# Kernel tuning notes

Measured on AMD Instinct MI355X. Metric: run time of the kernel, lower is better.

Reference implementation:

```python
import jax, jax.numpy as jnp
import numpy as np

N_FEATURES = 1024
N_HEADS = 16
D_ATTN = 64


def setup_inputs() -> dict:
    key = jax.random.key(0)
    k_x, k_qkv, k_pw, k_pb = jax.random.split(key, 4)
    B, S = 2, 2048
    x = jax.random.normal(k_x, (B, S, N_FEATURES), dtype=jnp.float32)
    # torch nn.Linear weights are [out, in]; init scale ~ 1/sqrt(in)
    w_qkv = jax.random.normal(k_qkv, (3 * N_HEADS * D_ATTN, N_FEATURES), dtype=jnp.float32) / np.sqrt(N_FEATURES)
    w_proj = jax.random.normal(k_pw, (N_FEATURES, N_HEADS * D_ATTN), dtype=jnp.float32) / np.sqrt(N_HEADS * D_ATTN)
    b_proj = jax.random.normal(k_pb, (N_FEATURES,), dtype=jnp.float32) / np.sqrt(N_HEADS * D_ATTN)
    return {"x": x, "w_qkv": w_qkv, "w_proj": w_proj, "b_proj": b_proj}


def reference(x, w_qkv, w_proj, b_proj):
    B, S, F = x.shape
    H, D = N_HEADS, D_ATTN
    # fused QKV projection (bias=False): [B,S,3*H*D]
    qkv = jnp.einsum('bsf,of->bso', x, w_qkv)
    qkv = qkv.reshape(B, S, 3, H, D)
    q = jnp.transpose(qkv[:, :, 0], (0, 2, 1, 3))  # [B,H,S,D]
    k = jnp.transpose(qkv[:, :, 1], (0, 2, 1, 3))
    v = jnp.transpose(qkv[:, :, 2], (0, 2, 1, 3))
    scale = 1.0 / jnp.sqrt(jnp.asarray(D, dtype=x.dtype))
    scores = jnp.einsum('bhqd,bhkd->bhqk', q, k) * scale  # [B,H,S,S]
    attn = jax.nn.softmax(scores, axis=-1)
    out = jnp.einsum('bhqk,bhkd->bhqd', attn, v)  # [B,H,S,D]
    out = jnp.transpose(out, (0, 2, 1, 3)).reshape(B, S, H * D)
    # output projection (dropout is identity in eval mode)
    return jnp.einsum('bsm,fm->bsf', out, w_proj) + b_proj
```

## Files before the change

kernel.cpp:

```cpp
#include <hip/hip_runtime.h>
#include <hip/hip_bf16.h>
#include <math.h>

#define BATCH 2
#define SEQ 2048
#define NFEAT 1024
#define NHEAD 16
#define DHEAD 64
#define MROWS (BATCH * SEQ)
#define NQKV (3 * NHEAD * DHEAD)

typedef __attribute__((ext_vector_type(8))) short short8;
typedef __attribute__((ext_vector_type(4))) float floatx4;
typedef __attribute__((ext_vector_type(16))) float floatx16;
typedef __attribute__((ext_vector_type(4))) unsigned int uintx4;

#define CEXP 0.18033688f

__device__ __forceinline__ unsigned short f2bf(float f) {
    unsigned int u = __float_as_uint(f);
    u += 0x7fff + ((u >> 16) & 1);
    return (unsigned short)(u >> 16);
}

__device__ __forceinline__ float fast_exp2(float x) {
    return __builtin_amdgcn_exp2f(x);
}

__device__ __forceinline__ uint pack_bf16x2(float lo, float hi) {
    float2 t; t.x = lo; t.y = hi;
    __hip_bfloat162 h = __float22bfloat162_rn(t);
    union { __hip_bfloat162 h; uint u; } c; c.h = h;
    return c.u;
}

__device__ __forceinline__ void async16(const void* g, void* l) {
    __builtin_amdgcn_global_load_lds(
        (const __attribute__((address_space(1))) void*)g,
        (__attribute__((address_space(3))) void*)l, 16, 0, 0);
}

#define BAR_RAW() asm volatile("s_barrier" ::: "memory")
#define WAITV4()  { asm volatile("s_waitcnt vmcnt(4)" ::: "memory"); __builtin_amdgcn_sched_barrier(0); }
#define WAITV0()  { asm volatile("s_waitcnt vmcnt(0)" ::: "memory"); __builtin_amdgcn_sched_barrier(0); }

__global__ void cvt_swz(const float* __restrict__ x, const float* __restrict__ wq,
                        const float* __restrict__ wp,
                        ushort* __restrict__ xb, ushort* __restrict__ wqb,
                        ushort* __restrict__ wpb) {
    const int NX = MROWS * NFEAT / 4, NWQ = NQKV * NFEAT / 4, NWP = NFEAT * NFEAT / 4;
    int i = blockIdx.x * blockDim.x + threadIdx.x;
    if (i >= NX + NWQ + NWP) return;
    const float* src; ushort* dst; int idx4;
    if (i < NX)            { src = x;  dst = xb;  idx4 = i; }
    else if (i < NX + NWQ) { src = wq; dst = wqb; idx4 = i - NX; }
    else                   { src = wp; dst = wpb; idx4 = i - NX - NWQ; }
    float4 v = ((const float4*)src)[idx4];
    ushort4 o;
    o.x = f2bf(v.x); o.y = f2bf(v.y); o.z = f2bf(v.z); o.w = f2bf(v.w);
    const int e = idx4 * 4;
    const int k = e & (NFEAT - 1);
    const int row = e >> 10;
    const int kp = (k & ~31) | (((((k >> 3) & 3) ^ ((row >> 1) & 3))) << 3) | (k & 7);
    *(ushort4*)(dst + (size_t)row * NFEAT + kp) = o;
}

__global__ __launch_bounds__(256, 3)
void gemm_qkv(const ushort* __restrict__ A, const ushort* __restrict__ W,
              ushort* __restrict__ qb, ushort* __restrict__ kb, ushort* __restrict__ vtb) {
    __shared__ ushort smem[16384];
    ushort* As = smem;
    ushort* Bs = smem + 8192;
    const int tid = threadIdx.x;
    const int wave = tid >> 6, lane = tid & 63;
    const int id = blockIdx.x;
    const int xcd = id & 7, slot = id >> 3;
    const int by = (xcd >> 1) * 8 + slot / 12;
    const int bx = (xcd & 1) * 12 + slot % 12;
    const int m0 = by * 128, n0 = bx * 128;
    const int wm = (wave >> 1) * 64, wn = (wave & 1) * 64;
    const int lr = lane & 15, lg = lane >> 4;
    const int kswz = (lg ^ ((lr >> 1) & 3)) * 8;

    floatx4 acc[4][4] = {};

    for (int k0 = 0; k0 < NFEAT; k0 += 64) {
#pragma unroll
        for (int q = 0; q < 4; ++q) {
            const int s = q * 256 + tid;
            const int row = s >> 3, kc = (s & 7) * 8;
            async16(A + (size_t)(m0 + row) * NFEAT + k0 + kc, (void*)(As + s * 8));
            async16(W + (size_t)(n0 + row) * NFEAT + k0 + kc, (void*)(Bs + s * 8));
        }
        __syncthreads();
#pragma unroll
        for (int kk = 0; kk < 2; ++kk) {
            short8 a[4], b[4];
#pragma unroll
            for (int i = 0; i < 4; ++i)
                a[i] = *(const short8*)(As + (wm + i * 16 + lr) * 64 + kk * 32 + kswz);
#pragma unroll
            for (int j = 0; j < 4; ++j)
                b[j] = *(const short8*)(Bs + (wn + j * 16 + lr) * 64 + kk * 32 + kswz);
#pragma unroll
            for (int i = 0; i < 4; ++i)
#pragma unroll
                for (int j = 0; j < 4; ++j)
                    acc[i][j] = __builtin_amdgcn_mfma_f32_16x16x32_bf16(a[i], b[j], acc[i][j], 0, 0, 0);
        }
        __syncthreads();
    }

    const int t = n0 >> 10;
    const int bidx = m0 >> 11;
    if (t < 2) {
#pragma unroll
        for (int i = 0; i < 4; ++i)
#pragma unroll
            for (int j = 0; j < 4; ++j)
#pragma unroll
                for (int r = 0; r < 4; ++r) {
                    const int m = m0 + wm + i * 16 + lg * 4 + r;
                    const int n = n0 + wn + j * 16 + lr;
                    const int s = m & (SEQ - 1);
                    const int rem = n & 1023, h = rem >> 6, d = rem & 63;
                    if (t == 0) {
                        qb[((size_t)(bidx * NHEAD + h) * SEQ + s) * DHEAD + d] =
                            f2bf(acc[i][j][r] * CEXP);
                    } else {
                        const int dcol = ((((d >> 3) ^ (s & 7)) << 3)) | (d & 7);
                        kb[((size_t)(bidx * NHEAD + h) * SEQ + s) * DHEAD + dcol] =
                            f2bf(acc[i][j][r]);
                    }
                }
    } else {
#pragma unroll
        for (int hhalf = 0; hhalf < 2; ++hhalf) {
            if ((wm >> 6) == hhalf) {
#pragma unroll
                for (int i = 0; i < 4; ++i) {
                    const int chunk = i * 2 + (lg >> 1);
#pragma unroll
                    for (int j = 0; j < 4; ++j) {
                        const int n = wn + j * 16 + lr;
                        uint2 pk;
                        pk.x = pack_bf16x2(acc[i][j][0], acc[i][j][1]);
                        pk.y = pack_bf16x2(acc[i][j][2], acc[i][j][3]);
                        *(uint2*)(smem + n * 64 + ((chunk ^ (n & 7)) * 8) + (lg & 1) * 4) = pk;
                    }
                }
            }
            __syncthreads();
            const int s_base = (m0 & (SEQ - 1)) + hhalf * 64;
#pragma unroll
            for (int it = 0; it < 4; ++it) {
                const int n_r = (tid >> 3) + it * 32;
                const int p = tid & 7;
                short8 rowv = *(const short8*)(smem + n_r * 64 + p * 8);
                const int nglob = n0 + n_r;
                const int d = nglob & 63, hh = (nglob & 1023) >> 6;
                *(short8*)(vtb + ((size_t)(bidx * NHEAD + hh) * DHEAD + d) * SEQ + s_base + p * 8) = rowv;
            }
            __syncthreads();
        }
    }
}

__global__ __launch_bounds__(256, 2)
void gemm_proj(const ushort* __restrict__ A, const ushort* __restrict__ W,
               const float* __restrict__ bias, float* __restrict__ Cout) {
    __shared__ ushort As[128 * 64];
    __shared__ ushort Bs[64 * 64];
    const int tid = threadIdx.x;
    const int wave = tid >> 6, lane = tid & 63;
    const int id = blockIdx.x;
    const int xcd = id & 7, slot = id >> 3;
    const int by = (xcd >> 1) * 8 + (slot >> 3);
    const int bx = (xcd & 1) * 8 + (slot & 7);
    const int m0 = by * 128, n0 = bx * 64;
    const int wm = (wave >> 1) * 64, wn = (wave & 1) * 32;
    const int lr = lane & 15, lg = lane >> 4;
    const int kswz = (lg ^ ((lr >> 1) & 3)) * 8;

    floatx4 acc[4][2] = {};

    for (int k0 = 0; k0 < NFEAT; k0 += 64) {
#pragma unroll
        for (int q = 0; q < 4; ++q) {
            const int s = q * 256 + tid;
            const int row = s >> 3, kc = (s & 7) * 8;
            async16(A + (size_t)(m0 + row) * NFEAT + k0 + kc, (void*)(As + s * 8));
        }
#pragma unroll
        for (int q = 0; q < 2; ++q) {
            const int s = q * 256 + tid;
            const int row = s >> 3, kc = (s & 7) * 8;
            async16(W + (size_t)(n0 + row) * NFEAT + k0 + kc, (void*)(Bs + s * 8));
        }
        __syncthreads();
#pragma unroll
        for (int kk = 0; kk < 2; ++kk) {
            short8 a[4], b[2];
#pragma unroll
            for (int i = 0; i < 4; ++i)
                a[i] = *(const short8*)(As + (wm + i * 16 + lr) * 64 + kk * 32 + kswz);
#pragma unroll
            for (int j = 0; j < 2; ++j)
                b[j] = *(const short8*)(Bs + (wn + j * 16 + lr) * 64 + kk * 32 + kswz);
#pragma unroll
            for (int i = 0; i < 4; ++i)
#pragma unroll
                for (int j = 0; j < 2; ++j)
                    acc[i][j] = __builtin_amdgcn_mfma_f32_16x16x32_bf16(a[i], b[j], acc[i][j], 0, 0, 0);
        }
        __syncthreads();
    }

#pragma unroll
    for (int i = 0; i < 4; ++i)
#pragma unroll
        for (int j = 0; j < 2; ++j)
#pragma unroll
            for (int r = 0; r < 4; ++r) {
                const int m = m0 + wm + i * 16 + lg * 4 + r;
                const int n = n0 + wn + j * 16 + lr;
                Cout[(size_t)m * NFEAT + n] = acc[i][j][r] + bias[n];
            }
}

__global__ __launch_bounds__(512, 4)
void flash_attn(const ushort* __restrict__ qb, const ushort* __restrict__ kb,
                const ushort* __restrict__ vtb, ushort* __restrict__ aob) {
    const int id = blockIdx.x;
    const int xcd = id & 7, slot = id >> 3;
    const int bh = xcd + 8 * (slot >> 4);
    const int qt = slot & 15;
    const int tid = threadIdx.x, wave = tid >> 6, lane = tid & 63;
    const int l31 = lane & 31, l5 = lane >> 5;
    const int swz = l31 & 7;
    const int kvh = wave >> 2;
    const int qw = wave & 3;

    __shared__ __align__(16) ushort sm[32768];
    ushort* Ksp = sm;
    ushort* Vsp = sm + 16384;

    const ushort* Qb = qb + (size_t)bh * SEQ * DHEAD;
    const ushort* Kb = kb + (size_t)bh * SEQ * DHEAD;
    const ushort* Vt = vtb + (size_t)bh * DHEAD * SEQ;

    const int q0 = qt * 128 + qw * 32;

    short8 qf[4];
#pragma unroll
    for (int kw = 0; kw < 4; ++kw)
        qf[kw] = *(const short8*)(Qb + (size_t)(q0 + l31) * DHEAD + kw * 16 + l5 * 8);

    const int kofs = tid * 8;
    const size_t vrow = (size_t)(tid >> 3) * SEQ;
    const int vcol = (tid & 7) * 8;

    const ushort* KsW = Ksp + kvh * 8192;
    const ushort* VsW = Vsp + kvh * 8192;

    floatx16 acc_o[2] = {};
    float l_lane = 0.0f;

#define FLASH_PREFETCH(BUF, KV)                                                     \
    {                                                                               \
        const int kv_ = (KV);                                                       \
        async16(Kb + (size_t)kv_ * DHEAD + kofs,          (void*)(Ksp + (BUF) * 4096 + kofs));        \
        async16(Kb + (size_t)(1024 + kv_) * DHEAD + kofs, (void*)(Ksp + 8192 + (BUF) * 4096 + kofs)); \
        async16(Vt + vrow + kv_ + vcol,                   (void*)(Vsp + (BUF) * 4096 + kofs));        \
        async16(Vt + vrow + 1024 + kv_ + vcol,            (void*)(Vsp + 8192 + (BUF) * 4096 + kofs)); \
    }

#define FLASH_COMPUTE(BUF)                                                          \
    {                                                                               \
        floatx16 st[2] = {};                                                        \
        __builtin_amdgcn_s_setprio(1);                                              \
        _Pragma("unroll")                                                           \
        for (int kw = 0; kw < 4; ++kw) {                                            \
            _Pragma("unroll")                                                       \
            for (int i = 0; i < 2; ++i) {                                           \
                short8 kf = *(const short8*)(KsW + (BUF) * 4096 + (i * 32 + l31) * 64 + \
                                             (((kw * 2 + l5) ^ swz) * 8));          \
                st[i] = __builtin_amdgcn_mfma_f32_32x32x16_bf16(kf, qf[kw], st[i], 0, 0, 0); \
            }                                                                       \
        }                                                                           \
        __builtin_amdgcn_s_setprio(0);                                              \
        uintx4 pa[4];                                                               \
        _Pragma("unroll")                                                           \
        for (int i = 0; i < 2; ++i) {                                               \
            uint P2[8];                                                             \
            float lsA = 0.0f, lsB = 0.0f;                                           \
            _Pragma("unroll")                                                       \
            for (int rr = 0; rr < 8; ++rr) {                                        \
                const float p0 = fast_exp2(st[i][rr * 2]);                          \
                const float p1 = fast_exp2(st[i][rr * 2 + 1]);                      \
                if (rr & 1) lsB += p0 + p1; else lsA += p0 + p1;                    \
                P2[rr] = pack_bf16x2(p0, p1);                                       \
            }                                                                       \
            l_lane += lsA + lsB;                                                    \
            _Pragma("unroll")                                                       \
            for (int r3 = 0; r3 < 2; ++r3) {                                        \
                _Pragma("unroll")                                                   \
                for (int r1 = 0; r1 < 2; ++r1) {                                    \
                    uint a = P2[r3 * 4 + r1];                            \
                    uint b = P2[r3 * 4 + 2 + r1];                        \
                    asm volatile("v_permlane32_swap_b32 %0, %1" : "+v"(a), "+v"(b)); \
                    pa[i * 2 + r3][r1] = a;               \
                    pa[i * 2 + r3][2 + r1] = b;           \
                }                                                                   \
            }                                                                       \
        }                                                                           \
        __builtin_amdgcn_s_setprio(1);                                              \
        _Pragma("unroll")                                                           \
        for (int kk = 0; kk < 4; ++kk) {                                            \
            const short8 paf = *(const short8*)&pa[kk];                             \
            _Pragma("unroll")                                                       \
            for (int j2 = 0; j2 < 2; ++j2) {                                        \
                short8 vf = *(const short8*)(VsW + (BUF) * 4096 + (j2 * 32 + l31) * 64 + \
                                             (((kk * 2 + l5) ^ swz) * 8));          \
                acc_o[j2] = __builtin_amdgcn_mfma_f32_32x32x16_bf16(paf, vf, acc_o[j2], 0, 0, 0); \
            }                                                                       \
        }                                                                           \
        __builtin_amdgcn_s_setprio(0);                                              \
    }

    FLASH_PREFETCH(0, 0)

    for (int kt = 0; kt < 1024; kt += 128) {
        BAR_RAW();
        FLASH_PREFETCH(1, kt + 64)
        WAITV4();
        BAR_RAW();
        FLASH_COMPUTE(0)
        BAR_RAW();
        if (kt + 128 < 1024) {
            FLASH_PREFETCH(0, kt + 128)
            WAITV4();
        } else {
            WAITV0();
        }
        BAR_RAW();
        FLASH_COMPUTE(1)
    }
#undef FLASH_PREFETCH
#undef FLASH_COMPUTE

    __syncthreads();
    float* mrg = (float*)sm;
    float* p = mrg + (size_t)(qw * 64 + lane) * 36;
    if (kvh == 1) {
#pragma unroll
        for (int j2 = 0; j2 < 2; ++j2)
#pragma unroll
            for (int r4 = 0; r4 < 4; ++r4) {
                floatx4 v;
                v[0] = acc_o[j2][r4 * 4 + 0];
                v[1] = acc_o[j2][r4 * 4 + 1];
                v[2] = acc_o[j2][r4 * 4 + 2];
                v[3] = acc_o[j2][r4 * 4 + 3];
                *(floatx4*)(p + j2 * 16 + r4 * 4) = v;
            }
        p[32] = l_lane;
    }
    __syncthreads();
    if (kvh == 0) {
#pragma unroll
        for (int j2 = 0; j2 < 2; ++j2)
#pragma unroll
            for (int r4 = 0; r4 < 4; ++r4) {
                floatx4 v = *(const floatx4*)(p + j2 * 16 + r4 * 4);
#pragma unroll
                for (int e = 0; e < 4; ++e)
                    acc_o[j2][r4 * 4 + e] += v[e];
            }
        l_lane += p[32];

        l_lane += __shfl_xor(l_lane, 32);
        const float invl = 1.0f / l_lane;

        const int b = bh >> 4, h = bh & 15;
#pragma unroll
        for (int r = 0; r < 16; ++r) {
            const int qrow = (r & 3) + 4 * l5 + 8 * (r >> 2);
            const float il = __shfl(invl, qrow);
            const int srow = b * SEQ + q0 + qrow;
            const int key = (srow >> 1) & 3;
#pragma unroll
            for (int j2 = 0; j2 < 2; ++j2) {
                const int d = j2 * 32 + l31;
                const int dsw = (d & ~31) | ((((d >> 3) & 3) ^ key) << 3) | (d & 7);
                aob[(size_t)srow * (NHEAD * DHEAD) + h * DHEAD + dsw] = f2bf(acc_o[j2][r] * il);
            }
        }
    }
}

extern "C" void kernel_launch(void* const* d_in, const int* in_sizes, int n_in,
                              void* d_out, int out_size, void* d_ws, size_t ws_size,
                              hipStream_t stream) {
    const float* x      = (const float*)d_in[0];
    const float* w_qkv  = (const float*)d_in[1];
    const float* w_proj = (const float*)d_in[2];
    const float* b_proj = (const float*)d_in[3];
    float* out = (float*)d_out;

    ushort* ws = (ushort*)d_ws;
    ushort* xb     = ws;
    ushort* wqkvb  = xb + (size_t)MROWS * NFEAT;
    ushort* wprojb = wqkvb + (size_t)NQKV * NFEAT;
    ushort* qb     = wprojb + (size_t)NFEAT * NFEAT;
    ushort* kb     = qb + (size_t)MROWS * NFEAT;
    ushort* vtb    = kb + (size_t)MROWS * NFEAT;
    ushort* aob    = vtb + (size_t)MROWS * NFEAT;

    {
        const int total = (MROWS * NFEAT + NQKV * NFEAT + NFEAT * NFEAT) / 4;
        cvt_swz<<<(total + 255) / 256, 256, 0, stream>>>(x, w_qkv, w_proj, xb, wqkvb, wprojb);
    }

    {
        gemm_qkv<<<768, 256, 0, stream>>>(xb, wqkvb, qb, kb, vtb);
    }

    {
        flash_attn<<<512, 512, 0, stream>>>(qb, kb, vtb, aob);
    }

    {
        gemm_proj<<<512, 256, 0, stream>>>(aob, wprojb, b_proj, out);
    }
}
```

Measured before the change: 178.0 us.

## Software-pipeline flash attention: overlap softmax of one tile with QK/PV MFMAs of next

Splits the per-tile flash step into separate QK, softmax and PV stages and reorders the loop so the QK matmul of tile k+1 and the PV matmul of tile k run back to back in one high-priority MFMA burst. Softmax then runs while the next async load is in flight. The intent is to hide exp/pack/permlane work and load latency behind matrix-core work. In exchange it keeps the st and pa buffers live across iterations, which raises register pressure, and adds a prologue and epilogue.

```diff
diff --git a/kernel.cpp b/kernel.cpp
--- a/kernel.cpp
+++ b/kernel.cpp
@@ -264,9 +264,11 @@
     const ushort* VsW = Vsp + kvh * 8192;
 
     floatx16 acc_o[2] = {};
+    floatx16 st[2];
+    uintx4 pa[4];
     float l_lane = 0.0f;
 
-#define FLASH_PREFETCH(BUF, KV)                                                     \
+#define S_STAGE(BUF, KV)                                                            \
     {                                                                               \
         const int kv_ = (KV);                                                       \
         async16(Kb + (size_t)kv_ * DHEAD + kofs,          (void*)(Ksp + (BUF) * 4096 + kofs));        \
@@ -275,10 +277,10 @@
         async16(Vt + vrow + 1024 + kv_ + vcol,            (void*)(Vsp + 8192 + (BUF) * 4096 + kofs)); \
     }
 
-#define FLASH_COMPUTE(BUF)                                                          \
+#define QK_STEP(BUF)                                                                \
     {                                                                               \
-        floatx16 st[2] = {};                                                        \
-        __builtin_amdgcn_s_setprio(1);                                              \
+        _Pragma("unroll")                                                           \
+        for (int e = 0; e < 16; ++e) { st[0][e] = 0.0f; st[1][e] = 0.0f; }          \
         _Pragma("unroll")                                                           \
         for (int kw = 0; kw < 4; ++kw) {                                            \
             _Pragma("unroll")                                                       \
@@ -288,8 +290,10 @@
                 st[i] = __builtin_amdgcn_mfma_f32_32x32x16_bf16(kf, qf[kw], st[i], 0, 0, 0); \
             }                                                                       \
         }                                                                           \
-        __builtin_amdgcn_s_setprio(0);                                              \
-        uintx4 pa[4];                                                               \
+    }
+
+#define SM_STEP()                                                                   \
+    {                                                                               \
         _Pragma("unroll")                                                           \
         for (int i = 0; i < 2; ++i) {                                               \
             uint P2[8];                                                             \
@@ -314,7 +318,10 @@
                 }                                                                   \
             }                                                                       \
         }                                                                           \
-        __builtin_amdgcn_s_setprio(1);                                              \
+    }
+
+#define PV_STEP(BUF)                                                                \
+    {                                                                               \
         _Pragma("unroll")                                                           \
         for (int kk = 0; kk < 4; ++kk) {                                            \
             const short8 paf = *(const short8*)&pa[kk];                             \
@@ -325,29 +332,49 @@
                 acc_o[j2] = __builtin_amdgcn_mfma_f32_32x32x16_bf16(paf, vf, acc_o[j2], 0, 0, 0); \
             }                                                                       \
         }                                                                           \
-        __builtin_amdgcn_s_setprio(0);                                              \
-    }
-
-    FLASH_PREFETCH(0, 0)
-
-    for (int kt = 0; kt < 1024; kt += 128) {
+    }
+
+    S_STAGE(0, 0)
+    S_STAGE(1, 64)
+    WAITV4();
+    BAR_RAW();
+    QK_STEP(0)
+    SM_STEP()
+
+    for (int kt = 0; kt < 14 * 64; kt += 128) {
+        WAITV0();
         BAR_RAW();
-        FLASH_PREFETCH(1, kt + 64)
-        WAITV4();
+        __builtin_amdgcn_s_setprio(1);
+        QK_STEP(1)
+        PV_STEP(0)
+        __builtin_amdgcn_s_setprio(0);
         BAR_RAW();
-        FLASH_COMPUTE(0)
+        S_STAGE(0, kt + 128)
+        SM_STEP()
+        WAITV0();
         BAR_RAW();
-        if (kt + 128 < 1024) {
-            FLASH_PREFETCH(0, kt + 128)
-            WAITV4();
-        } else {
-            WAITV0();
-        }
+        __builtin_amdgcn_s_setprio(1);
+        QK_STEP(0)
+        PV_STEP(1)
+        __builtin_amdgcn_s_setprio(0);
         BAR_RAW();
-        FLASH_COMPUTE(1)
-    }
-#undef FLASH_PREFETCH
-#undef FLASH_COMPUTE
+        S_STAGE(1, kt + 192)
+        SM_STEP()
+    }
+    WAITV0();
+    BAR_RAW();
+    __builtin_amdgcn_s_setprio(1);
+    QK_STEP(1)
+    PV_STEP(0)
+    __builtin_amdgcn_s_setprio(0);
+    SM_STEP()
+    __builtin_amdgcn_s_setprio(1);
+    PV_STEP(1)
+    __builtin_amdgcn_s_setprio(0);
+#undef S_STAGE
+#undef QK_STEP
+#undef SM_STEP
+#undef PV_STEP
 
     __syncthreads();
     float* mrg = (float*)sm;
```

After: 221.9 us. 24.6% more time.
